# Performance work log

Measured on AMD Instinct MI355X. Metric: run time of the kernel, lower is better.

## Reference

```python
import math
import jax, jax.numpy as jnp
import numpy as np

NUM_HEADS = 12
NUM_GROUPS = 12
NUM_BUCKETS = 32
MAX_DISTANCE = 128
EPS_GN = 1e-5
EPS_LN = 1e-5


def _layernorm(x, w, b):
    mu = x.mean(axis=-1, keepdims=True)
    xc = x - mu
    inv = jax.lax.rsqrt((xc * xc).mean(axis=-1, keepdims=True) + EPS_LN)
    return xc * inv * w + b


def _rel_pos_bias(T, emb):
    # T5-style bucketed relative position bias -> (1, n_heads, T, T)
    ctx = jnp.arange(T)[:, None]
    mem = jnp.arange(T)[None, :]
    n = -(mem - ctx)  # = context - memory
    nb = NUM_BUCKETS // 2  # bidirectional
    ret = (n < 0).astype(jnp.int32) * nb
    n = jnp.abs(n)
    max_exact = nb // 2
    val_large = max_exact + (
        jnp.log(jnp.maximum(n, 1).astype(jnp.float32) / max_exact)
        / math.log(MAX_DISTANCE / max_exact) * (nb - max_exact)
    ).astype(jnp.int32)
    val_large = jnp.minimum(val_large, nb - 1)
    bucket = ret + jnp.where(n < max_exact, n, val_large)  # (T, T)
    vals = emb[bucket]  # (T, T, He)
    return jnp.transpose(vals, (2, 0, 1))[None]  # (1, He, T, T)


def setup_inputs() -> dict:
    key = jax.random.key(0)
    ks = jax.random.split(key, 12)
    T, B, C, H, W, D = 64, 1, 768, 8, 8, 8
    hd = C // NUM_HEADS
    return {
        "x": jax.random.normal(ks[0], (T, B, C, H, W, D), jnp.float32),
        "norm1_w": jax.random.normal(ks[1], (C,), jnp.float32),
        "w_in": jax.random.normal(ks[2], (3 * C, C), jnp.float32) * 0.02,
        "b_in": jax.random.normal(ks[3], (3 * C,), jnp.float32) * 0.02,
        "qn_w": jax.random.normal(ks[4], (hd,), jnp.float32),
        "qn_b": jnp.zeros((hd,), jnp.float32),
        "kn_w": jax.random.normal(ks[5], (hd,), jnp.float32),
        "kn_b": jnp.zeros((hd,), jnp.float32),
        "rel_emb": jax.random.normal(ks[6], (NUM_BUCKETS, NUM_HEADS), jnp.float32),
        "w_out": jax.random.normal(ks[7], (C, C), jnp.float32) * 0.02,
        "b_out": jax.random.normal(ks[8], (C,), jnp.float32) * 0.02,
        "gamma": jax.random.normal(ks[9], (C,), jnp.float32) * 1e-6,
    }


def reference(x, norm1_w, w_in, b_in, qn_w, qn_b, kn_w, kn_b, rel_emb, w_out, b_out, gamma):
    T, B, C, H, W, D = x.shape
    He = NUM_HEADS
    hd = C // He
    xt = x.reshape(T * B, C, H, W, D)

    # RMSGroupNorm (actually standard group_norm, weight only, no bias)
    xg = xt.reshape(T * B, NUM_GROUPS, C // NUM_GROUPS, H, W, D)
    mu = xg.mean(axis=(2, 3, 4, 5), keepdims=True)
    var = ((xg - mu) ** 2).mean(axis=(2, 3, 4, 5), keepdims=True)
    xn = (xg - mu) * jax.lax.rsqrt(var + EPS_GN)
    xn = xn.reshape(T * B, C, H, W, D) * norm1_w[None, :, None, None, None]

    # 1x1x1 Conv3d input head == per-voxel linear
    qkv = jnp.einsum('ncxyz,oc->noxyz', xn, w_in) + b_in[None, :, None, None, None]

    # rearrange '(t b) (he c) h w d -> (b h w d) he t c'
    qkv = qkv.reshape(T, B, He, 3 * hd, H, W, D)
    qkv = jnp.transpose(qkv, (1, 4, 5, 6, 2, 0, 3)).reshape(B * H * W * D, He, T, 3 * hd)
    q, k, v = jnp.split(qkv, 3, axis=-1)
    q = _layernorm(q, qn_w, qn_b)
    k = _layernorm(k, kn_w, kn_b)

    bias = _rel_pos_bias(T, rel_emb)  # (1, He, T, T)
    scores = jnp.einsum('nhtc,nhsc->nhts', q, k) / math.sqrt(hd) + bias
    att = jax.nn.softmax(scores, axis=-1)
    o = jnp.einsum('nhts,nhsc->nhtc', att, v)  # (BHWD, He, T, hd)

    # rearrange '(b h w d) he t c -> (t b) (he c) h w d'
    o = o.reshape(B, H, W, D, He, T, hd)
    o = jnp.transpose(o, (5, 0, 4, 6, 1, 2, 3)).reshape(T * B, C, H, W, D)

    o = jnp.einsum('ncxyz,oc->noxyz', o, w_out) + b_out[None, :, None, None, None]
    o = o.reshape(T, B, C, H, W, D)

    # layer-scale residual (drop_path = identity)
    return x + gamma[None, None, :, None, None, None] * o
```

## Files before the change

kernel.cpp:

```cpp
#include <hip/hip_runtime.h>


typedef unsigned int u32;
typedef unsigned short u16;
typedef __attribute__((ext_vector_type(4))) float f32x4;
typedef __attribute__((ext_vector_type(8))) short s16x8;

__device__ __forceinline__ float bfl(u32 w){ union{u32 i; float f;} u; u.i = w<<16; return u.f; }
__device__ __forceinline__ float bfh(u32 w){ union{u32 i; float f;} u; u.i = w & 0xffff0000u; return u.f; }
__device__ __forceinline__ u16 f2bf(float f){ union{float ff; u32 i;} u; u.ff = f; u32 r = u.i + 0x7fffu + ((u.i>>16)&1u); return (u16)(r>>16); }
__device__ __forceinline__ u32 pk2(float a, float b){ return (u32)f2bf(a) | ((u32)f2bf(b)<<16); }

__device__ __forceinline__ void gll16(const u16* g, u16* l){
  __builtin_amdgcn_global_load_lds((const __attribute__((address_space(1))) void*)g,
                                   (__attribute__((address_space(3))) void*)l, 16, 0, 0);
}

__global__ void k_bias(const float* __restrict__ rel, float* __restrict__ bias_d){
  int d = threadIdx.x;
  if (d < 127){
    int delta = d - 63;
    int ret = (delta < 0) ? 16 : 0;
    int a = delta < 0 ? -delta : delta;
    int bkt;
    if (a < 8) bkt = a;
    else {
      float lr = (logf((float)a * 0.125f) / logf(16.0f)) * 8.0f;
      int vl = 8 + (int)lr;
      bkt = vl > 15 ? 15 : vl;
    }
    bkt += ret;
    for (int he = 0; he < 12; ++he) bias_d[he*128 + d] = rel[bkt*12 + he];
  }
}

__global__ void k_cast(const float* __restrict__ a, const float* __restrict__ b,
                       u16* __restrict__ ab, u16* __restrict__ bb){
  const int n1 = 2304*768, n2 = 768*768;
  for (int i = blockIdx.x*blockDim.x + threadIdx.x; i < n1+n2; i += gridDim.x*blockDim.x){
    if (i < n1) ab[i] = f2bf(a[i]);
    else        bb[i-n1] = f2bf(b[i-n1]);
  }
}

__global__ __launch_bounds__(256) void k_stats(const float* __restrict__ x, float* __restrict__ stats){
  __shared__ float red[8];
  const float4* xb = (const float4*)(x + (size_t)blockIdx.x * 32768);
  float s = 0.f, s2 = 0.f;
  for (int i = threadIdx.x; i < 8192; i += 256){
    float4 v = xb[i];
    s  += v.x + v.y + v.z + v.w;
    s2 += v.x*v.x + v.y*v.y + v.z*v.z + v.w*v.w;
  }
  #pragma unroll
  for (int off = 32; off; off >>= 1){ s += __shfl_down(s, off); s2 += __shfl_down(s2, off); }
  int wid = threadIdx.x >> 6;
  if ((threadIdx.x & 63) == 0){ red[wid*2] = s; red[wid*2+1] = s2; }
  __syncthreads();
  if (threadIdx.x == 0){
    float ts = 0.f, ts2 = 0.f;
    for (int w = 0; w < 4; ++w){ ts += red[w*2]; ts2 += red[w*2+1]; }
    float mu  = ts * (1.f/32768.f);
    float var = ts2 * (1.f/32768.f) - mu*mu;
    stats[blockIdx.x*2]   = mu;
    stats[blockIdx.x*2+1] = rsqrtf(var + 1e-5f);
  }
}

__global__ __launch_bounds__(256) void k_norm(const float* __restrict__ x, const float* __restrict__ stats,
                                              const float* __restrict__ w1, u16* __restrict__ xnT){
  __shared__ float ld[64][65];
  const int b = blockIdx.x;
  const int tb = b / 96, rem = b % 96, cb = rem >> 3, vb = rem & 7;
  const float mu  = stats[(tb*12+cb)*2];
  const float inv = stats[(tb*12+cb)*2+1];
  const int tid = threadIdx.x;
  #pragma unroll
  for (int it = 0; it < 4; ++it){
    int chunk = it*256 + tid;
    int cl = chunk >> 4, v4 = chunk & 15;
    float w = w1[cb*64 + cl] * inv;
    float4 v = *(const float4*)(x + ((size_t)(tb*768 + cb*64 + cl)*512 + vb*64 + v4*4));
    ld[cl][v4*4+0] = (v.x - mu) * w;
    ld[cl][v4*4+1] = (v.y - mu) * w;
    ld[cl][v4*4+2] = (v.z - mu) * w;
    ld[cl][v4*4+3] = (v.w - mu) * w;
  }
  __syncthreads();
  #pragma unroll
  for (int it = 0; it < 2; ++it){
    int chunk = it*256 + tid;
    int vl = chunk >> 3, p = chunk & 7;
    u32 ow[4];
    #pragma unroll
    for (int j = 0; j < 4; ++j)
      ow[j] = pk2(ld[p*8 + j*2][vl], ld[p*8 + j*2 + 1][vl]);
    uint4 q4; q4.x = ow[0]; q4.y = ow[1]; q4.z = ow[2]; q4.w = ow[3];
    *(uint4*)(xnT + ((size_t)(tb*512 + vb*64 + vl)*768 + cb*64 + p*8)) = q4;
  }
}

__global__ __launch_bounds__(256) void k_gemm(const u16* __restrict__ At, const u16* __restrict__ Bt,
    const int M, const int K, const int mtiles, const int epi,
    const float* __restrict__ bias, u16* __restrict__ outT,
    const float* __restrict__ xres, const float* __restrict__ gamma,
    const float* __restrict__ bout, float* __restrict__ outp)
{
  __shared__ u16 lta[128*32];
  __shared__ u16 ltb[128*32];
  const int tid = threadIdx.x;
  const int l = tid & 63;
  const int wid = tid >> 6;
  const int wm = wid & 1, wn = wid >> 1;
  const int mt = blockIdx.x % mtiles, nt = blockIdx.x / mtiles;
  const f32x4 z = {0.f, 0.f, 0.f, 0.f};
  f32x4 acc[4][4];
  #pragma unroll
  for (int i = 0; i < 4; ++i)
    #pragma unroll
    for (int j = 0; j < 4; ++j) acc[i][j] = z;
  const int nk = K >> 5;
  const int sr = tid >> 2, sq = tid & 3;
  const u16* gA = At + (size_t)(mt*128 + sr)*K + sq*8;
  const u16* gB = Bt + (size_t)(nt*128 + sr)*K + sq*8;
  u16* lA0 = lta + wid*512;
  u16* lA1 = lta + 2048 + wid*512;
  u16* lB0 = ltb + wid*512;
  u16* lB1 = ltb + 2048 + wid*512;
  for (int kt = 0; kt < nk; ++kt){
    __syncthreads();
    gll16(gA + kt*32,              lA0);
    gll16(gA + kt*32 + (size_t)64*K, lA1);
    gll16(gB + kt*32,              lB0);
    gll16(gB + kt*32 + (size_t)64*K, lB1);
    __syncthreads();
    s16x8 fa[4], fb[4];
    #pragma unroll
    for (int f = 0; f < 4; ++f){
      fa[f] = *(const s16x8*)&ltb[(wn*64 + f*16 + (l&15))*32 + ((l>>4)<<3)];
      fb[f] = *(const s16x8*)&lta[(wm*64 + f*16 + (l&15))*32 + ((l>>4)<<3)];
    }
    #pragma unroll
    for (int fn = 0; fn < 4; ++fn)
      #pragma unroll
      for (int fm = 0; fm < 4; ++fm)
        acc[fn][fm] = __builtin_amdgcn_mfma_f32_16x16x32_bf16(fa[fn], fb[fm], acc[fn][fm], 0, 0, 0);
  }
  const int rsub = (l>>4) << 2, cbase = l & 15;
  if (epi == 1){
    #pragma unroll
    for (int fn = 0; fn < 4; ++fn)
      #pragma unroll
      for (int fm = 0; fm < 4; ++fm){
        const int n0 = nt*128 + wn*64 + fn*16 + rsub;
        const int m  = mt*128 + wm*64 + fm*16 + cbase;
        const float bm = bias[m];
        #pragma unroll
        for (int r = 0; r < 4; ++r)
          outT[(size_t)(n0 + r)*M + m] = f2bf(acc[fn][fm][r] + bm);
      }
  } else {
    #pragma unroll
    for (int fn = 0; fn < 4; ++fn)
      #pragma unroll
      for (int fm = 0; fm < 4; ++fm){
        const int n0 = nt*128 + wn*64 + fn*16 + rsub;
        const int m  = mt*128 + wm*64 + fm*16 + cbase;
        const int t = n0 >> 9, vox = n0 & 511;
        const size_t idx = ((size_t)t*768 + m)*512 + vox;
        const float gm = gamma[m], bo = bout[m];
        const float4 xv = *(const float4*)(xres + idx);
        float4 ov;
        ov.x = xv.x + gm*(acc[fn][fm][0] + bo);
        ov.y = xv.y + gm*(acc[fn][fm][1] + bo);
        ov.z = xv.z + gm*(acc[fn][fm][2] + bo);
        ov.w = xv.w + gm*(acc[fn][fm][3] + bo);
        *(float4*)(outp + idx) = ov;
      }
  }
}

__device__ __forceinline__ void ln8(uint4 v, const float* wv, const float* bv, u16* dst){
  float e[8];
  const u32* p = (const u32*)&v;
  #pragma unroll
  for (int j = 0; j < 4; ++j){ e[2*j] = bfl(p[j]); e[2*j+1] = bfh(p[j]); }
  float s = 0.f, s2 = 0.f;
  #pragma unroll
  for (int j = 0; j < 8; ++j){ s += e[j]; s2 += e[j]*e[j]; }
  #pragma unroll
  for (int off = 1; off < 8; off <<= 1){ s += __shfl_xor(s, off); s2 += __shfl_xor(s2, off); }
  float mu  = s * (1.f/64.f);
  float inv = rsqrtf(s2*(1.f/64.f) - mu*mu + 1e-5f);
  u32 ow[4];
  #pragma unroll
  for (int j = 0; j < 4; ++j)
    ow[j] = pk2((e[2*j]-mu)*inv*wv[2*j] + bv[2*j],
                (e[2*j+1]-mu)*inv*wv[2*j+1] + bv[2*j+1]);
  uint4 q4; q4.x = ow[0]; q4.y = ow[1]; q4.z = ow[2]; q4.w = ow[3];
  *(uint4*)dst = q4;
}

__global__ __launch_bounds__(256) void k_attn(const u16* __restrict__ qkvT, const float* __restrict__ bias_d,
    const float* __restrict__ qn_w, const float* __restrict__ qn_b,
    const float* __restrict__ kn_w, const float* __restrict__ kn_b,
    u16* __restrict__ oT)
{
  __shared__ u16 qt[64][72], ktl[64][72], vtl[64][72];
  __shared__ float bd[128];
  const int tid = threadIdx.x;
  const int w = tid >> 6, l = tid & 63;
  const int he = blockIdx.x % 12;
  const int vox = blockIdx.x / 12;
  if (tid < 127) bd[tid] = bias_d[he*128 + tid];
  const int c0 = (l & 7) * 8;
  const int rl = l >> 3;
  float qwv[8], qbv[8], kwv[8], kbv[8];
  *(float4*)&qwv[0] = *(const float4*)(qn_w + c0); *(float4*)&qwv[4] = *(const float4*)(qn_w + c0 + 4);
  *(float4*)&qbv[0] = *(const float4*)(qn_b + c0); *(float4*)&qbv[4] = *(const float4*)(qn_b + c0 + 4);
  *(float4*)&kwv[0] = *(const float4*)(kn_w + c0); *(float4*)&kwv[4] = *(const float4*)(kn_w + c0 + 4);
  *(float4*)&kbv[0] = *(const float4*)(kn_b + c0); *(float4*)&kbv[4] = *(const float4*)(kn_b + c0 + 4);
  #pragma unroll
  for (int i = 0; i < 2; ++i){
    const int r = w*16 + i*8 + rl;
    const u16* gb = qkvT + ((size_t)(r*512 + vox))*2304 + he*192 + c0;
    uint4 qv = *(const uint4*)(gb);
    uint4 kv = *(const uint4*)(gb + 64);
    uint4 vv = *(const uint4*)(gb + 128);
    ln8(qv, qwv, qbv, &qt[r][c0]);
    ln8(kv, kwv, kbv, &ktl[r][c0]);
    const u32* p = (const u32*)&vv;
    #pragma unroll
    for (int j = 0; j < 4; ++j){
      vtl[c0 + 2*j][r]     = (u16)(p[j] & 0xffffu);
      vtl[c0 + 2*j + 1][r] = (u16)(p[j] >> 16);
    }
  }
  __syncthreads();
  const int lc = l & 15, lh = l >> 4;
  const f32x4 z = {0.f, 0.f, 0.f, 0.f};
  f32x4 sa[4] = {z, z, z, z};
  #pragma unroll
  for (int ks = 0; ks < 2; ++ks){
    s16x8 fq = *(const s16x8*)&qt[w*16 + lc][ks*32 + lh*8];
    #pragma unroll
    for (int fc = 0; fc < 4; ++fc){
      s16x8 fk = *(const s16x8*)&ktl[fc*16 + lc][ks*32 + lh*8];
      sa[fc] = __builtin_amdgcn_mfma_f32_16x16x32_bf16(fq, fk, sa[fc], 0, 0, 0);
    }
  }
  u16 (*pt)[72] = qt;
  const int rsub = lh << 2;
  #pragma unroll
  for (int r = 0; r < 4; ++r){
    const int row = w*16 + rsub + r;
    float v0 = sa[0][r]*0.125f + bd[row - lc      + 63];
    float v1 = sa[1][r]*0.125f + bd[row - lc - 16 + 63];
    float v2 = sa[2][r]*0.125f + bd[row - lc - 32 + 63];
    float v3 = sa[3][r]*0.125f + bd[row - lc - 48 + 63];
    float m = fmaxf(fmaxf(v0, v1), fmaxf(v2, v3));
    #pragma unroll
    for (int off = 1; off < 16; off <<= 1) m = fmaxf(m, __shfl_xor(m, off));
    v0 = __expf(v0 - m); v1 = __expf(v1 - m); v2 = __expf(v2 - m); v3 = __expf(v3 - m);
    float sum = v0 + v1 + v2 + v3;
    #pragma unroll
    for (int off = 1; off < 16; off <<= 1) sum += __shfl_xor(sum, off);
    float rs = 1.0f / sum;
    pt[row][lc]      = f2bf(v0*rs);
    pt[row][lc + 16] = f2bf(v1*rs);
    pt[row][lc + 32] = f2bf(v2*rs);
    pt[row][lc + 48] = f2bf(v3*rs);
  }
  asm volatile("s_waitcnt lgkmcnt(0)" ::: "memory");
  __builtin_amdgcn_sched_barrier(0);
  f32x4 oa[4] = {z, z, z, z};
  #pragma unroll
  for (int ks = 0; ks < 2; ++ks){
    s16x8 fp = *(const s16x8*)&pt[w*16 + lc][ks*32 + lh*8];
    #pragma unroll
    for (int fc = 0; fc < 4; ++fc){
      s16x8 fv = *(const s16x8*)&vtl[fc*16 + lc][ks*32 + lh*8];
      oa[fc] = __builtin_amdgcn_mfma_f32_16x16x32_bf16(fp, fv, oa[fc], 0, 0, 0);
    }
  }
  #pragma unroll
  for (int fc = 0; fc < 4; ++fc){
    const int c = fc*16 + lc;
    #pragma unroll
    for (int r = 0; r < 4; ++r){
      const int t = w*16 + rsub + r;
      oT[((size_t)(t*512 + vox))*768 + he*64 + c] = f2bf(oa[fc][r]);
    }
  }
}

extern "C" void kernel_launch(void* const* d_in, const int* in_sizes, int n_in,
                              void* d_out, int out_size, void* d_ws, size_t ws_size,
                              hipStream_t stream) {
  (void)in_sizes; (void)n_in; (void)out_size; (void)ws_size;
  const float* x      = (const float*)d_in[0];
  const float* norm1w = (const float*)d_in[1];
  const float* w_in   = (const float*)d_in[2];
  const float* b_in   = (const float*)d_in[3];
  const float* qn_w   = (const float*)d_in[4];
  const float* qn_b   = (const float*)d_in[5];
  const float* kn_w   = (const float*)d_in[6];
  const float* kn_b   = (const float*)d_in[7];
  const float* rel    = (const float*)d_in[8];
  const float* w_out  = (const float*)d_in[9];
  const float* b_out  = (const float*)d_in[10];
  const float* gamma  = (const float*)d_in[11];
  float* out = (float*)d_out;

  char* ws = (char*)d_ws;
  float* stats  = (float*)(ws + 0);
  float* bias_d = (float*)(ws + 6144);
  u16*   winb   = (u16*)(ws + 12288);
  u16*   woutb  = (u16*)(ws + 3551232);
  u16*   xnT    = (u16*)(ws + 4730880);
  u16*   oT     = xnT;
  u16*   qkvT   = (u16*)(ws + 55062528);

  k_bias <<<1,    128, 0, stream>>>(rel, bias_d);
  k_cast <<<2048, 256, 0, stream>>>(w_in, w_out, winb, woutb);
  k_stats<<<768,  256, 0, stream>>>(x, stats);
  k_norm <<<6144, 256, 0, stream>>>(x, stats, norm1w, xnT);
  k_gemm <<<4608, 256, 0, stream>>>(winb, xnT, 2304, 768, 18, 1,
                                    b_in, qkvT, nullptr, nullptr, nullptr, nullptr);
  k_attn <<<6144, 256, 0, stream>>>(qkvT, bias_d, qn_w, qn_b, kn_w, kn_b, oT);
  k_gemm <<<1536, 256, 0, stream>>>(woutb, oT, 768, 768, 6, 2,
                                    nullptr, nullptr, x, gamma, b_out, out);
}
```

Measured before the change: 574.0 us.

## Rewrite GEMM with 256x256 tiles, double-buffered LDS, swizzle and XCD remap

Replaces the 128x128 single-buffered GEMM with a 512-thread 256x256 tile kernel. It double-buffers the LDS stages so the next K slice loads while the current one computes, and uses a single barrier per iteration. It also XOR-swizzles LDS chunks to avoid bank conflicts and remaps block IDs across the 8 XCDs for cache locality. The QKV epilogue now writes packed vector stores. The larger tile raises register and LDS pressure and yields fewer blocks.

```diff
diff --git a/kernel.cpp b/kernel.cpp
--- a/kernel.cpp
+++ b/kernel.cpp
@@ -100,83 +100,117 @@
   }
 }
 
-__global__ __launch_bounds__(256) void k_gemm(const u16* __restrict__ At, const u16* __restrict__ Bt,
-    const int M, const int K, const int mtiles, const int epi,
+template<int EPI>
+__global__ __launch_bounds__(512, 2) void k_gemm256(
+    const u16* __restrict__ At, const u16* __restrict__ Bt,
+    const int M, const int mtiles,
     const float* __restrict__ bias, u16* __restrict__ outT,
     const float* __restrict__ xres, const float* __restrict__ gamma,
     const float* __restrict__ bout, float* __restrict__ outp)
 {
-  __shared__ u16 lta[128*32];
-  __shared__ u16 ltb[128*32];
+  __shared__ u16 lds[2][2][8192];
+  const int K = 768, nkt = 24;
   const int tid = threadIdx.x;
-  const int l = tid & 63;
-  const int wid = tid >> 6;
+  const int l = tid & 63, wid = tid >> 6;
   const int wm = wid & 1, wn = wid >> 1;
-  const int mt = blockIdx.x % mtiles, nt = blockIdx.x / mtiles;
+  const int cpx = gridDim.x >> 3;
+  const int wg = (blockIdx.x & 7) * cpx + (blockIdx.x >> 3);
+  const int mt = wg % mtiles, nt = wg / mtiles;
+
+  const int srow = tid >> 2;
+  const int cg = (tid ^ (tid >> 3)) & 3;
+  const u16* gA = At + (size_t)(mt*256 + srow)*K + cg*8;
+  const u16* gB = Bt + (size_t)(nt*256 + srow)*K + cg*8;
+
+  const int cSwz = ((l>>4) ^ (l>>1)) & 3;
+  const int aoff = (wm*128 + (l&15))*32 + cSwz*8;
+  const int boff = (wn*64  + (l&15))*32 + cSwz*8;
+
+  f32x4 acc[8][4];
   const f32x4 z = {0.f, 0.f, 0.f, 0.f};
-  f32x4 acc[4][4];
-  #pragma unroll
-  for (int i = 0; i < 4; ++i)
+  #pragma unroll
+  for (int i = 0; i < 8; ++i)
     #pragma unroll
     for (int j = 0; j < 4; ++j) acc[i][j] = z;
-  const int nk = K >> 5;
-  const int sr = tid >> 2, sq = tid & 3;
-  const u16* gA = At + (size_t)(mt*128 + sr)*K + sq*8;
-  const u16* gB = Bt + (size_t)(nt*128 + sr)*K + sq*8;
-  u16* lA0 = lta + wid*512;
-  u16* lA1 = lta + 2048 + wid*512;
-  u16* lB0 = ltb + wid*512;
-  u16* lB1 = ltb + 2048 + wid*512;
-  for (int kt = 0; kt < nk; ++kt){
-    __syncthreads();
-    gll16(gA + kt*32,              lA0);
-    gll16(gA + kt*32 + (size_t)64*K, lA1);
-    gll16(gB + kt*32,              lB0);
-    gll16(gB + kt*32 + (size_t)64*K, lB1);
-    __syncthreads();
-    s16x8 fa[4], fb[4];
-    #pragma unroll
-    for (int f = 0; f < 4; ++f){
-      fa[f] = *(const s16x8*)&ltb[(wn*64 + f*16 + (l&15))*32 + ((l>>4)<<3)];
-      fb[f] = *(const s16x8*)&lta[(wm*64 + f*16 + (l&15))*32 + ((l>>4)<<3)];
-    }
-    #pragma unroll
-    for (int fn = 0; fn < 4; ++fn)
+
+  #define STAGE(slot, kt) do { \
+    u16* la = &lds[slot][0][0] + tid*8; \
+    u16* lb = &lds[slot][1][0] + tid*8; \
+    gll16(gA + (kt)*32,                 la); \
+    gll16(gA + (kt)*32 + (size_t)128*K, la + 4096); \
+    gll16(gB + (kt)*32,                 lb); \
+    gll16(gB + (kt)*32 + (size_t)128*K, lb + 4096); \
+  } while(0)
+
+  STAGE(0, 0);
+  asm volatile("s_waitcnt vmcnt(0)" ::: "memory");
+  __builtin_amdgcn_s_barrier();
+  __builtin_amdgcn_sched_barrier(0);
+
+  for (int kt = 0; kt < nkt; ++kt){
+    const int slot = kt & 1;
+    if (kt + 1 < nkt) STAGE(slot ^ 1, kt + 1);
+    const u16* Ab = &lds[slot][0][0];
+    const u16* Bb = &lds[slot][1][0];
+    s16x8 fa[8], fb[4];
+    #pragma unroll
+    for (int mf = 0; mf < 8; ++mf) fa[mf] = *(const s16x8*)(Ab + aoff + mf*512);
+    #pragma unroll
+    for (int nf = 0; nf < 4; ++nf) fb[nf] = *(const s16x8*)(Bb + boff + nf*512);
+    #pragma unroll
+    for (int mf = 0; mf < 8; ++mf)
       #pragma unroll
-      for (int fm = 0; fm < 4; ++fm)
-        acc[fn][fm] = __builtin_amdgcn_mfma_f32_16x16x32_bf16(fa[fn], fb[fm], acc[fn][fm], 0, 0, 0);
-  }
-  const int rsub = (l>>4) << 2, cbase = l & 15;
-  if (epi == 1){
-    #pragma unroll
-    for (int fn = 0; fn < 4; ++fn)
+      for (int nf = 0; nf < 4; ++nf){
+        if (EPI == 1)
+          acc[mf][nf] = __builtin_amdgcn_mfma_f32_16x16x32_bf16(fa[mf], fb[nf], acc[mf][nf], 0, 0, 0);
+        else
+          acc[mf][nf] = __builtin_amdgcn_mfma_f32_16x16x32_bf16(fb[nf], fa[mf], acc[mf][nf], 0, 0, 0);
+      }
+    if (kt + 1 < nkt){
+      asm volatile("s_waitcnt vmcnt(0)" ::: "memory");
+      __builtin_amdgcn_s_barrier();
+      __builtin_amdgcn_sched_barrier(0);
+    }
+  }
+  #undef STAGE
+
+  if (EPI == 1){
+    const int nbase = nt*256 + wn*64 + (l & 15);
+    const int mbase = mt*256 + wm*128 + ((l >> 4) << 2);
+    #pragma unroll
+    for (int mf = 0; mf < 8; ++mf){
+      const int m0 = mbase + mf*16;
+      const float4 b4 = *(const float4*)(bias + m0);
       #pragma unroll
-      for (int fm = 0; fm < 4; ++fm){
-        const int n0 = nt*128 + wn*64 + fn*16 + rsub;
-        const int m  = mt*128 + wm*64 + fm*16 + cbase;
-        const float bm = bias[m];
-        #pragma unroll
-        for (int r = 0; r < 4; ++r)
-          outT[(size_t)(n0 + r)*M + m] = f2bf(acc[fn][fm][r] + bm);
+      for (int nf = 0; nf < 4; ++nf){
+        const int n = nbase + nf*16;
+        uint2 u;
+        u.x = pk2(acc[mf][nf][0] + b4.x, acc[mf][nf][1] + b4.y);
+        u.y = pk2(acc[mf][nf][2] + b4.z, acc[mf][nf][3] + b4.w);
+        *(uint2*)(outT + (size_t)n*M + m0) = u;
       }
+    }
   } else {
-    #pragma unroll
-    for (int fn = 0; fn < 4; ++fn)
+    const int nbase = nt*256 + wn*64 + ((l >> 4) << 2);
+    const int mbase = mt*256 + wm*128 + (l & 15);
+    #pragma unroll
+    for (int mf = 0; mf < 8; ++mf){
+      const int m = mbase + mf*16;
+      const float gm = gamma[m], bo = bout[m];
       #pragma unroll
-      for (int fm = 0; fm < 4; ++fm){
-        const int n0 = nt*128 + wn*64 + fn*16 + rsub;
-        const int m  = mt*128 + wm*64 + fm*16 + cbase;
+      for (int nf = 0; nf < 4; ++nf){
+        const int n0 = nbase + nf*16;
         const int t = n0 >> 9, vox = n0 & 511;
         const size_t idx = ((size_t)t*768 + m)*512 + vox;
-        const float gm = gamma[m], bo = bout[m];
         const float4 xv = *(const float4*)(xres + idx);
         float4 ov;
-        ov.x = xv.x + gm*(acc[fn][fm][0] + bo);
-        ov.y = xv.y + gm*(acc[fn][fm][1] + bo);
-        ov.z = xv.z + gm*(acc[fn][fm][2] + bo);
-        ov.w = xv.w + gm*(acc[fn][fm][3] + bo);
+        ov.x = xv.x + gm*(acc[mf][nf][0] + bo);
+        ov.y = xv.y + gm*(acc[mf][nf][1] + bo);
+        ov.z = xv.z + gm*(acc[mf][nf][2] + bo);
+        ov.w = xv.w + gm*(acc[mf][nf][3] + bo);
         *(float4*)(outp + idx) = ov;
       }
+    }
   }
 }
 
@@ -325,9 +359,9 @@
   k_cast <<<2048, 256, 0, stream>>>(w_in, w_out, winb, woutb);
   k_stats<<<768,  256, 0, stream>>>(x, stats);
   k_norm <<<6144, 256, 0, stream>>>(x, stats, norm1w, xnT);
-  k_gemm <<<4608, 256, 0, stream>>>(winb, xnT, 2304, 768, 18, 1,
-                                    b_in, qkvT, nullptr, nullptr, nullptr, nullptr);
+  k_gemm256<1><<<1152, 512, 0, stream>>>(winb, xnT, 2304, 9,
+                                         b_in, qkvT, nullptr, nullptr, nullptr, nullptr);
   k_attn <<<6144, 256, 0, stream>>>(qkvT, bias_d, qn_w, qn_b, kn_w, kn_b, oT);
-  k_gemm <<<1536, 256, 0, stream>>>(woutb, oT, 768, 768, 6, 2,
-                                    nullptr, nullptr, x, gamma, b_out, out);
-}
+  k_gemm256<2><<<384, 512, 0, stream>>>(woutb, oT, 768, 3,
+                                        nullptr, nullptr, x, gamma, b_out, out);
+}
```

After: 538.3 us. 1.07x faster.
